# Kernel optimization log

Hardware: AMD Instinct MI355X
Metric: run time of the kernel (lower is better)

Reference implementation:

```python
import jax, jax.numpy as jnp
import numpy as np

WS = 7          # window size hardcoded in the module
NUM_HEADS = 8
IN_DIM = 512
BATCH = 2048


def _relative_position_index(ws=WS):
    # Mirrors the torch meshgrid ('ij') construction in __init__.
    coords = np.stack(np.meshgrid(np.arange(ws), np.arange(ws), indexing='ij'))  # [2, ws, ws]
    cf = coords.reshape(2, -1)                        # [2, ws*ws]
    rel = cf[:, :, None] - cf[:, None, :]             # [2, N, N]
    rel = rel.transpose(1, 2, 0).copy()               # [N, N, 2]
    rel[:, :, 0] += ws - 1
    rel[:, :, 1] += ws - 1
    rel[:, :, 0] *= 2 * ws - 1
    return rel.sum(-1).astype(np.int32)               # [N, N]


def setup_inputs() -> dict:
    key = jax.random.key(0)
    k1, k2, k3, k4 = jax.random.split(key, 4)
    C = IN_DIM
    x = jax.random.normal(k1, (BATCH, C, WS, WS), dtype=jnp.float32)
    # 1x1 convs are channel matmuls; store squeezed [out, in] weights.
    qkv_w = jax.random.normal(k2, (3 * C, C), dtype=jnp.float32) * 0.02
    proj_w = jax.random.normal(k3, (C, C), dtype=jnp.float32) * 0.02
    proj_b = jnp.zeros((C,), dtype=jnp.float32)
    bias_table = jax.random.normal(k4, ((2 * WS - 1) ** 2, NUM_HEADS), dtype=jnp.float32) * 0.02
    rel_index = jnp.asarray(_relative_position_index())
    return {"x": x, "qkv_w": qkv_w, "proj_w": proj_w, "proj_b": proj_b,
            "bias_table": bias_table, "rel_index": rel_index}


def reference(x, qkv_w, proj_w, proj_b, bias_table, rel_index):
    B, C, H, W = x.shape
    N = H * W
    h = NUM_HEADS
    d = C // h
    scale = d ** (-0.5)

    xf = x.reshape(B, C, N)
    # qkv 1x1 conv -> [B, 3C, N] -> [B, 3, h, d, N]
    qkv = jnp.einsum('oc,bcn->bon', qkv_w, xf).reshape(B, 3, h, d, N)
    # torch permute(1,0,2,4,3): q,k,v each [B, h, N, d]
    q = qkv[:, 0].transpose(0, 1, 3, 2)
    k = qkv[:, 1].transpose(0, 1, 3, 2)
    v = qkv[:, 2].transpose(0, 1, 3, 2)

    attn = jnp.einsum('bhnd,bhmd->bhnm', q, k) * scale  # [B, h, N, N]
    bias = bias_table[rel_index.reshape(-1)].reshape(N, N, h).transpose(2, 0, 1)  # [h, N, N]
    attn = jax.nn.softmax(attn + bias[None], axis=-1)

    out = jnp.einsum('bhnm,bhmd->bhnd', attn, v)        # [B, h, N, d]
    # torch: transpose(2,3).reshape(B, C, H, W) -> [B, h, d, N] flattened over (h, d)
    out = out.transpose(0, 1, 3, 2).reshape(B, C, H, W)
    out = jnp.einsum('oc,bchw->bohw', proj_w, out) + proj_b[None, :, None, None]
    return out
```

## Files before the change

kernel.cpp:

```cpp
#include <hip/hip_runtime.h>
#include <hip/hip_bf16.h>
#include <stdint.h>


#define BATCH 2048
#define CIN 512
#define NTOK 49
#define NHEAD 8

typedef __attribute__((ext_vector_type(4))) float    ffrag;
typedef __attribute__((ext_vector_type(8))) _Float16 hfrag;
typedef __attribute__((ext_vector_type(4))) float    f32x4;

#define WQKV_BYTES  (1536*512*2)
#define WPROJ_OFF   ((size_t)WQKV_BYTES)
#define WPROJ_BYTES (512*512*2)
#define BIAS_OFF    (WPROJ_OFF + WPROJ_BYTES)
#define BIAS_BYTES  (8*64*64*4)

__global__ void prep_kernel(const float* __restrict__ qkv_w,
                            const float* __restrict__ proj_w,
                            const float* __restrict__ bias_table,
                            const int*   __restrict__ rel_index,
                            _Float16* __restrict__ wqkv,
                            _Float16* __restrict__ wproj,
                            float*    __restrict__ biasf) {
    int idx = blockIdx.x * blockDim.x + threadIdx.x;
    const int NQ = 1536*512;
    const int NP = 512*512;
    if (idx < NQ) {
        wqkv[idx] = (_Float16)qkv_w[idx];
    } else if (idx < NQ + NP) {
        int i = idx - NQ;
        wproj[i] = (_Float16)proj_w[i];
    } else if (idx < NQ + NP + 8*64*64) {
        int i = idx - NQ - NP;
        int h = i >> 12;
        int n = (i >> 6) & 63;
        int m = i & 63;
        float v;
        if (m >= NTOK)      v = -1e9f;
        else if (n >= NTOK) v = 0.0f;
        else                v = bias_table[rel_index[n*NTOK + m]*NHEAD + h];
        biasf[i] = v;
    }
}

__global__ __launch_bounds__(512, 2) void mhsa_fused_kernel(
        const float* __restrict__ x,
        const _Float16* __restrict__ wqkv,
        const _Float16* __restrict__ wproj,
        const float* __restrict__ projb,
        const float* __restrict__ biasf,
        float* __restrict__ out) {
    extern __shared__ char lds[];
    char* xsT = lds;

    const int b    = blockIdx.x;
    const int tid  = threadIdx.x;
    const int wid  = tid >> 6;
    const int lane = tid & 63;
    const int l15  = lane & 15;
    const int g    = lane >> 4;
    char* tile = lds + 65536 + (wid << 13);

    {
        const int c = tid;
        const float* xc = x + (size_t)b * (CIN*NTOK) + (size_t)c * NTOK;
        const int cb = c << 1;
        #pragma unroll 7
        for (int t = 0; t < NTOK; ++t)
            *(_Float16*)(xsT + t*1024 + (cb ^ ((t&7)<<4))) = (_Float16)xc[t];
        #pragma unroll
        for (int t = NTOK; t < 64; ++t)
            *(_Float16*)(xsT + t*1024 + (cb ^ ((t&7)<<4))) = (_Float16)0.0f;
    }
    __syncthreads();

    const int h = wid;
    hfrag qa[8], kb[8], pa[8], vb[8];

    auto read_frags = [&](hfrag* dst) {
        #pragma unroll
        for (int mt = 0; mt < 4; ++mt)
            #pragma unroll
            for (int ksp = 0; ksp < 2; ++ksp)
                dst[mt*2+ksp] = *(const hfrag*)(tile + (16*mt + l15)*128 +
                                  ((ksp*64 + g*16) ^ ((l15&7)<<4)));
    };

    auto qkv_pass = [&](int s, int trans) {
        ffrag acc[4][4];
        #pragma unroll
        for (int nt = 0; nt < 4; ++nt)
            #pragma unroll
            for (int mt = 0; mt < 4; ++mt) { ffrag z = {0.f,0.f,0.f,0.f}; acc[nt][mt] = z; }

        const _Float16* wb = wqkv + ((size_t)(s*512 + h*64 + l15))*512 + g*8;
        hfrag Bf[2][4];
        #pragma unroll
        for (int nt = 0; nt < 4; ++nt)
            Bf[0][nt] = *(const hfrag*)(wb + nt*8192);

        #pragma unroll
        for (int ks = 0; ks < 16; ++ks) {
            if (ks < 15) {
                #pragma unroll
                for (int nt = 0; nt < 4; ++nt)
                    Bf[(ks+1)&1][nt] = *(const hfrag*)(wb + nt*8192 + (ks+1)*32);
            }
            hfrag Af[4];
            #pragma unroll
            for (int mt = 0; mt < 4; ++mt)
                Af[mt] = *(const hfrag*)(xsT + (16*mt + l15)*1024 +
                           ((ks*64 + g*16) ^ ((l15&7)<<4)));
            #pragma unroll
            for (int nt = 0; nt < 4; ++nt)
                #pragma unroll
                for (int mt = 0; mt < 4; ++mt)
                    acc[nt][mt] = __builtin_amdgcn_mfma_f32_16x16x32_f16(
                        Af[mt], Bf[ks&1][nt], acc[nt][mt], 0, 0, 0);
        }
        #pragma unroll
        for (int nt = 0; nt < 4; ++nt)
            #pragma unroll
            for (int mt = 0; mt < 4; ++mt)
                #pragma unroll
                for (int i = 0; i < 4; ++i) {
                    int tok = 16*mt + 4*g + i;
                    int d   = 16*nt + l15;
                    _Float16 v = (_Float16)acc[nt][mt][i];
                    if (!trans)
                        *(_Float16*)(tile + tok*128 + ((2*d) ^ ((tok&7)<<4))) = v;
                    else
                        *(_Float16*)(tile + d*128 + ((2*tok) ^ ((d&7)<<4))) = v;
                }
    };

    qkv_pass(0, 0);  read_frags(qa);
    qkv_pass(1, 0);  read_frags(kb);

    ffrag sacc[4][4];
    #pragma unroll
    for (int nt = 0; nt < 4; ++nt)
        #pragma unroll
        for (int mt = 0; mt < 4; ++mt) { ffrag z = {0.f,0.f,0.f,0.f}; sacc[nt][mt] = z; }
    #pragma unroll
    for (int nt = 0; nt < 4; ++nt)
        #pragma unroll
        for (int mt = 0; mt < 4; ++mt)
            #pragma unroll
            for (int ksp = 0; ksp < 2; ++ksp)
                sacc[nt][mt] = __builtin_amdgcn_mfma_f32_16x16x32_f16(
                    qa[mt*2+ksp], kb[nt*2+ksp], sacc[nt][mt], 0, 0, 0);

    const float* bh = biasf + (h << 12);
    #pragma unroll
    for (int nt = 0; nt < 4; ++nt)
        #pragma unroll
        for (int mt = 0; mt < 4; ++mt)
            #pragma unroll
            for (int i = 0; i < 4; ++i) {
                int n = 16*mt + 4*g + i, m = 16*nt + l15;
                sacc[nt][mt][i] = sacc[nt][mt][i]*0.125f + bh[(n<<6) + m];
            }

    float rmax[4][4], rsum[4][4];
    #pragma unroll
    for (int mt = 0; mt < 4; ++mt)
        #pragma unroll
        for (int i = 0; i < 4; ++i)
            rmax[mt][i] = fmaxf(fmaxf(sacc[0][mt][i], sacc[1][mt][i]),
                                fmaxf(sacc[2][mt][i], sacc[3][mt][i]));
    #pragma unroll
    for (int off = 1; off <= 8; off <<= 1)
        #pragma unroll
        for (int mt = 0; mt < 4; ++mt)
            #pragma unroll
            for (int i = 0; i < 4; ++i)
                rmax[mt][i] = fmaxf(rmax[mt][i], __shfl_xor(rmax[mt][i], off));
    #pragma unroll
    for (int mt = 0; mt < 4; ++mt)
        #pragma unroll
        for (int i = 0; i < 4; ++i) rsum[mt][i] = 0.0f;
    #pragma unroll
    for (int nt = 0; nt < 4; ++nt)
        #pragma unroll
        for (int mt = 0; mt < 4; ++mt)
            #pragma unroll
            for (int i = 0; i < 4; ++i) {
                float p = __expf(sacc[nt][mt][i] - rmax[mt][i]);
                sacc[nt][mt][i] = p;
                rsum[mt][i] += p;
            }
    #pragma unroll
    for (int off = 1; off <= 8; off <<= 1)
        #pragma unroll
        for (int mt = 0; mt < 4; ++mt)
            #pragma unroll
            for (int i = 0; i < 4; ++i)
                rsum[mt][i] += __shfl_xor(rsum[mt][i], off);

    #pragma unroll
    for (int nt = 0; nt < 4; ++nt)
        #pragma unroll
        for (int mt = 0; mt < 4; ++mt)
            #pragma unroll
            for (int i = 0; i < 4; ++i) {
                int n = 16*mt + 4*g + i, m = 16*nt + l15;
                *(_Float16*)(tile + n*128 + ((2*m) ^ ((n&7)<<4))) = (_Float16)sacc[nt][mt][i];
            }
    read_frags(pa);

    float inv[4][4];
    #pragma unroll
    for (int mt = 0; mt < 4; ++mt)
        #pragma unroll
        for (int i = 0; i < 4; ++i) inv[mt][i] = 1.0f / rsum[mt][i];

    qkv_pass(2, 1);  read_frags(vb);

    ffrag oacc[4][4];
    #pragma unroll
    for (int dt = 0; dt < 4; ++dt)
        #pragma unroll
        for (int mt = 0; mt < 4; ++mt) { ffrag z = {0.f,0.f,0.f,0.f}; oacc[dt][mt] = z; }
    #pragma unroll
    for (int dt = 0; dt < 4; ++dt)
        #pragma unroll
        for (int mt = 0; mt < 4; ++mt)
            #pragma unroll
            for (int ksp = 0; ksp < 2; ++ksp)
                oacc[dt][mt] = __builtin_amdgcn_mfma_f32_16x16x32_f16(
                    pa[mt*2+ksp], vb[dt*2+ksp], oacc[dt][mt], 0, 0, 0);

    __syncthreads();
    #pragma unroll
    for (int dt = 0; dt < 4; ++dt)
        #pragma unroll
        for (int mt = 0; mt < 4; ++mt)
            #pragma unroll
            for (int i = 0; i < 4; ++i) {
                int tok = 16*mt + 4*g + i;
                int ch  = (h<<6) + 16*dt + l15;
                float v = oacc[dt][mt][i] * inv[mt][i];
                *(_Float16*)(xsT + tok*1024 + ((2*ch) ^ ((tok&7)<<4))) = (_Float16)v;
            }
    __syncthreads();

    {
        ffrag acc[4][4];
        #pragma unroll
        for (int nt = 0; nt < 4; ++nt)
            #pragma unroll
            for (int mt = 0; mt < 4; ++mt) { ffrag z = {0.f,0.f,0.f,0.f}; acc[nt][mt] = z; }

        const _Float16* wb = wproj + ((size_t)((wid<<6) + l15))*512 + g*8;
        hfrag Bf[2][4];
        #pragma unroll
        for (int nt = 0; nt < 4; ++nt)
            Bf[0][nt] = *(const hfrag*)(wb + nt*8192);

        #pragma unroll
        for (int ks = 0; ks < 16; ++ks) {
            if (ks < 15) {
                #pragma unroll
                for (int nt = 0; nt < 4; ++nt)
                    Bf[(ks+1)&1][nt] = *(const hfrag*)(wb + nt*8192 + (ks+1)*32);
            }
            hfrag Af[4];
            #pragma unroll
            for (int mt = 0; mt < 4; ++mt)
                Af[mt] = *(const hfrag*)(xsT + (16*mt + l15)*1024 +
                           ((ks*64 + g*16) ^ ((l15&7)<<4)));
            #pragma unroll
            for (int nt = 0; nt < 4; ++nt)
                #pragma unroll
                for (int mt = 0; mt < 4; ++mt)
                    acc[nt][mt] = __builtin_amdgcn_mfma_f32_16x16x32_f16(
                        Af[mt], Bf[ks&1][nt], acc[nt][mt], 0, 0, 0);
        }

        #pragma unroll
        for (int nt = 0; nt < 4; ++nt) {
            int o = (wid<<6) + 16*nt + l15;
            float pb = projb[o];
            float* op = out + ((size_t)b*512 + o)*NTOK;
            #pragma unroll
            for (int mt = 0; mt < 4; ++mt)
                #pragma unroll
                for (int i = 0; i < 4; ++i) {
                    int n = 16*mt + 4*g + i;
                    if (n < NTOK) op[n] = acc[nt][mt][i] + pb;
                }
        }
    }
}

extern "C" void kernel_launch(void* const* d_in, const int* in_sizes, int n_in,
                              void* d_out, int out_size, void* d_ws, size_t ws_size,
                              hipStream_t stream) {
    const float* x      = (const float*)d_in[0];
    const float* qkv_w  = (const float*)d_in[1];
    const float* proj_w = (const float*)d_in[2];
    const float* proj_b = (const float*)d_in[3];
    const float* bias_t = (const float*)d_in[4];
    const int*   rel    = (const int*)d_in[5];
    float* out = (float*)d_out;

    char* ws = (char*)d_ws;
    _Float16* wqkv  = (_Float16*)(ws);
    _Float16* wproj = (_Float16*)(ws + WPROJ_OFF);
    float*    biasf = (float*)(ws + BIAS_OFF);

    (void)hipFuncSetAttribute((const void*)mhsa_fused_kernel,
                              hipFuncAttributeMaxDynamicSharedMemorySize,
                              131072);

    const int prep_total = 1536*512 + 512*512 + 8*64*64;
    prep_kernel<<<(prep_total + 255)/256, 256, 0, stream>>>(
        qkv_w, proj_w, bias_t, rel, wqkv, wproj, biasf);
    mhsa_fused_kernel<<<BATCH, 512, 131072, stream>>>(
        x, wqkv, wproj, proj_b, biasf, out);
}
```

Before: 990.9 us.

## Pre-transpose input to fp16 in a separate kernel and halve fused kernel LDS

```diff
diff --git a/kernel.cpp b/kernel.cpp
--- a/kernel.cpp
+++ b/kernel.cpp
@@ -11,12 +11,14 @@
 typedef __attribute__((ext_vector_type(4))) float    ffrag;
 typedef __attribute__((ext_vector_type(8))) _Float16 hfrag;
 typedef __attribute__((ext_vector_type(4))) float    f32x4;
+typedef __attribute__((ext_vector_type(4), aligned(4))) float f32x4u;
 
 #define WQKV_BYTES  (1536*512*2)
 #define WPROJ_OFF   ((size_t)WQKV_BYTES)
 #define WPROJ_BYTES (512*512*2)
 #define BIAS_OFF    (WPROJ_OFF + WPROJ_BYTES)
 #define BIAS_BYTES  (8*64*64*4)
+#define XT_OFF      (BIAS_OFF + BIAS_BYTES)
 
 __global__ void prep_kernel(const float* __restrict__ qkv_w,
                             const float* __restrict__ proj_w,
@@ -46,15 +48,47 @@
     }
 }
 
-__global__ __launch_bounds__(512, 2) void mhsa_fused_kernel(
-        const float* __restrict__ x,
+__global__ __launch_bounds__(256) void transpose_kernel(
+        const float* __restrict__ x, _Float16* __restrict__ xT) {
+    __shared__ char lbuf[65536];
+    const int b   = blockIdx.x;
+    const int tid = threadIdx.x;
+
+    const f32x4* xb = (const f32x4*)(x + (size_t)b * (CIN*NTOK));
+    #pragma unroll
+    for (int it = 0; it < 25; ++it) {
+        int f4 = tid + it*256;
+        if (f4 < 6272) {
+            f32x4 v = xb[f4];
+            int base = f4 * 4;
+            #pragma unroll
+            for (int e = 0; e < 4; ++e) {
+                int idx = base + e;
+                int c = idx / NTOK;
+                int n = idx - c*NTOK;
+                *(_Float16*)(lbuf + n*1024 + ((c*2) ^ ((n&7)<<4))) = (_Float16)v[e];
+            }
+        }
+    }
+    for (int i = tid; i < 3840; i += 256)
+        *(uint32_t*)(lbuf + 50176 + i*4) = 0u;
+    __syncthreads();
+
+    const f32x4* src = (const f32x4*)lbuf;
+    f32x4*       dst = (f32x4*)(xT + (size_t)b * 32768);
+    #pragma unroll
+    for (int it = 0; it < 16; ++it)
+        dst[tid + it*256] = src[tid + it*256];
+}
+
+__global__ __launch_bounds__(512, 4) void mhsa_fused_kernel(
+        const _Float16* __restrict__ xT,
         const _Float16* __restrict__ wqkv,
         const _Float16* __restrict__ wproj,
         const float* __restrict__ projb,
         const float* __restrict__ biasf,
         float* __restrict__ out) {
     extern __shared__ char lds[];
-    char* xsT = lds;
 
     const int b    = blockIdx.x;
     const int tid  = threadIdx.x;
@@ -62,20 +96,8 @@
     const int lane = tid & 63;
     const int l15  = lane & 15;
     const int g    = lane >> 4;
-    char* tile = lds + 65536 + (wid << 13);
-
-    {
-        const int c = tid;
-        const float* xc = x + (size_t)b * (CIN*NTOK) + (size_t)c * NTOK;
-        const int cb = c << 1;
-        #pragma unroll 7
-        for (int t = 0; t < NTOK; ++t)
-            *(_Float16*)(xsT + t*1024 + (cb ^ ((t&7)<<4))) = (_Float16)xc[t];
-        #pragma unroll
-        for (int t = NTOK; t < 64; ++t)
-            *(_Float16*)(xsT + t*1024 + (cb ^ ((t&7)<<4))) = (_Float16)0.0f;
-    }
-    __syncthreads();
+    char* tile = lds + (wid << 13);
+    const char* xw = (const char*)(xT + (size_t)b * 32768);
 
     const int h = wid;
     hfrag qa[8], kb[8], pa[8], vb[8];
@@ -112,7 +134,7 @@
             hfrag Af[4];
             #pragma unroll
             for (int mt = 0; mt < 4; ++mt)
-                Af[mt] = *(const hfrag*)(xsT + (16*mt + l15)*1024 +
+                Af[mt] = *(const hfrag*)(xw + (16*mt + l15)*1024 +
                            ((ks*64 + g*16) ^ ((l15&7)<<4)));
             #pragma unroll
             for (int nt = 0; nt < 4; ++nt)
@@ -234,7 +256,6 @@
                 oacc[dt][mt] = __builtin_amdgcn_mfma_f32_16x16x32_f16(
                     pa[mt*2+ksp], vb[dt*2+ksp], oacc[dt][mt], 0, 0, 0);
 
-    __syncthreads();
     #pragma unroll
     for (int dt = 0; dt < 4; ++dt)
         #pragma unroll
@@ -242,9 +263,9 @@
             #pragma unroll
             for (int i = 0; i < 4; ++i) {
                 int tok = 16*mt + 4*g + i;
-                int ch  = (h<<6) + 16*dt + l15;
+                int d   = 16*dt + l15;
                 float v = oacc[dt][mt][i] * inv[mt][i];
-                *(_Float16*)(xsT + tok*1024 + ((2*ch) ^ ((tok&7)<<4))) = (_Float16)v;
+                *(_Float16*)(tile + tok*128 + ((2*d) ^ ((tok&7)<<4))) = (_Float16)v;
             }
     __syncthreads();
 
@@ -269,10 +290,15 @@
                     Bf[(ks+1)&1][nt] = *(const hfrag*)(wb + nt*8192 + (ks+1)*32);
             }
             hfrag Af[4];
-            #pragma unroll
-            for (int mt = 0; mt < 4; ++mt)
-                Af[mt] = *(const hfrag*)(xsT + (16*mt + l15)*1024 +
-                           ((ks*64 + g*16) ^ ((l15&7)<<4)));
+            {
+                const int c0 = ks*32 + g*8;
+                const char* tb = lds + ((c0 >> 6) << 13);
+                const int doff = 2*(c0 & 63);
+                #pragma unroll
+                for (int mt = 0; mt < 4; ++mt)
+                    Af[mt] = *(const hfrag*)(tb + (16*mt + l15)*128 +
+                               (doff ^ ((l15&7)<<4)));
+            }
             #pragma unroll
             for (int nt = 0; nt < 4; ++nt)
                 #pragma unroll
@@ -287,12 +313,14 @@
             float pb = projb[o];
             float* op = out + ((size_t)b*512 + o)*NTOK;
             #pragma unroll
-            for (int mt = 0; mt < 4; ++mt)
-                #pragma unroll
-                for (int i = 0; i < 4; ++i) {
-                    int n = 16*mt + 4*g + i;
-                    if (n < NTOK) op[n] = acc[nt][mt][i] + pb;
-                }
+            for (int mt = 0; mt < 3; ++mt) {
+                f32x4u v4;
+                #pragma unroll
+                for (int i = 0; i < 4; ++i) v4[i] = acc[nt][mt][i] + pb;
+                *(f32x4u*)(op + 16*mt + 4*g) = v4;
+            }
+            if (g == 0)
+                op[48] = acc[nt][3][0] + pb;
         }
     }
 }
@@ -312,14 +340,16 @@
     _Float16* wqkv  = (_Float16*)(ws);
     _Float16* wproj = (_Float16*)(ws + WPROJ_OFF);
     float*    biasf = (float*)(ws + BIAS_OFF);
+    _Float16* xT    = (_Float16*)(ws + XT_OFF);
 
     (void)hipFuncSetAttribute((const void*)mhsa_fused_kernel,
                               hipFuncAttributeMaxDynamicSharedMemorySize,
-                              131072);
+                              65536);
 
     const int prep_total = 1536*512 + 512*512 + 8*64*64;
     prep_kernel<<<(prep_total + 255)/256, 256, 0, stream>>>(
         qkv_w, proj_w, bias_t, rel, wqkv, wproj, biasf);
-    mhsa_fused_kernel<<<BATCH, 512, 131072, stream>>>(
-        x, wqkv, wproj, proj_b, biasf, out);
+    transpose_kernel<<<BATCH, 256, 0, stream>>>(x, xT);
+    mhsa_fused_kernel<<<BATCH, 512, 65536, stream>>>(
+        xT, wqkv, wproj, proj_b, biasf, out);
 }
```

Measured after the change: 3.048 ms. +207.6%, slower.
